# Performance work log

Measured on AMD Instinct MI355X. Metric: run time of the kernel, lower is better.

The kernel has to match this reference:

```python
import jax, jax.numpy as jnp
import numpy as np

INPUT_DIM = 1024
HIDDEN_DIM = 2048
NUM_BLOCKS = 8
BLOCK_SIZE = HIDDEN_DIM // NUM_BLOCKS
BATCH = 2048


def setup_inputs() -> dict:
    key = jax.random.key(0)
    ks = jax.random.split(key, 6)
    # PyTorch GRUCell init: uniform(-1/sqrt(hidden_size), 1/sqrt(hidden_size))
    bound = 1.0 / np.sqrt(BLOCK_SIZE)
    u = lambda k, shape: jax.random.uniform(k, shape, jnp.float32, -bound, bound)
    return {
        "input": jax.random.normal(ks[0], (BATCH, INPUT_DIM), jnp.float32),
        "hidden": jax.random.normal(ks[1], (BATCH, HIDDEN_DIM), jnp.float32),
        # stacked per-block GRUCell params (block-diagonal structure)
        "W_ih": u(ks[2], (NUM_BLOCKS, 3 * BLOCK_SIZE, INPUT_DIM)),
        "W_hh": u(ks[3], (NUM_BLOCKS, 3 * BLOCK_SIZE, BLOCK_SIZE)),
        "b_ih": u(ks[4], (NUM_BLOCKS, 3 * BLOCK_SIZE)),
        "b_hh": u(ks[5], (NUM_BLOCKS, 3 * BLOCK_SIZE)),
    }


def reference(input, hidden, W_ih, W_hh, b_ih, b_hh):
    B = input.shape[0]
    nb, g3, bs = W_hh.shape  # [num_blocks, 3*block_size, block_size]
    hb = hidden.reshape(B, nb, bs)                      # [B, nb, bs]
    # input-to-gate and hidden-to-gate projections, batched over blocks
    gi = jnp.einsum("bi,ngi->bng", input, W_ih) + b_ih  # [B, nb, 3*bs]
    gh = jnp.einsum("bns,ngs->bng", hb, W_hh) + b_hh    # [B, nb, 3*bs]
    i_r, i_z, i_n = jnp.split(gi, 3, axis=-1)
    h_r, h_z, h_n = jnp.split(gh, 3, axis=-1)
    r = jax.nn.sigmoid(i_r + h_r)
    z = jax.nn.sigmoid(i_z + h_z)
    n = jnp.tanh(i_n + r * h_n)
    new_h = (1.0 - z) * n + z * hb                      # [B, nb, bs]
    return new_h.reshape(B, nb * bs)
```

## Files before the change

### kernel.cpp

```cpp
#include <hip/hip_runtime.h>
#include <hip/hip_bf16.h>
#include <type_traits>

typedef __attribute__((ext_vector_type(4))) float f32x4;
typedef __attribute__((ext_vector_type(8))) short bf16x8;

template <int V> using ic = std::integral_constant<int, V>;

static constexpr int B_   = 2048;
static constexpr int IN_  = 1024;
static constexpr int HID_ = 2048;
static constexpr int NB_  = 8;
static constexpr int BS_  = 256;
static constexpr int G3_  = 768;

__device__ __forceinline__ unsigned cvtpk(float lo, float hi) {
  unsigned r;
  asm("v_cvt_pk_bf16_f32 %0, %1, %2" : "=v"(r) : "v"(lo), "v"(hi));
  return r;
}

__global__ __launch_bounds__(256, 2) void gru_mfma(
    const float* __restrict__ xf,
    const float* __restrict__ hf,
    const float* __restrict__ Wih,
    const float* __restrict__ Whh,
    const float* __restrict__ b_ih,
    const float* __restrict__ b_hh,
    float* __restrict__ out)
{
  __shared__ __align__(16) char lds[2][40960];

  const int t    = threadIdx.x;
  const int lane = t & 63;
  const int wid  = t >> 6;
  const int wm   = wid >> 1;
  const int wn   = wid & 1;

  const int bid = blockIdx.x;
  const int swz = (bid & 7) * 64 + (bid >> 3);
  const int mrow0 = (swz & 15) * 128;
  const int ct    = swz >> 4;
  const int n     = ct >> 2;
  const int s0    = (ct & 3) * 64;

  int arow[4], acol[4];
#pragma unroll
  for (int p = 0; p < 4; ++p) {
    int op = p * 4096 + t * 16;
    int ol = op ^ (((op >> 7) & 7) << 4);
    arow[p] = ol >> 7;
    acol[p] = (ol & 127) >> 1;
  }
  int wgrow[6], wcol[6];
#pragma unroll
  for (int q = 0; q < 6; ++q) {
    int op = q * 4096 + t * 16;
    int ol = op ^ (((op >> 7) & 7) << 4);
    int wr = ol >> 7;
    wgrow[q] = n * G3_ + (wr >> 6) * BS_ + s0 + (wr & 63);
    wcol[q]  = (ol & 127) >> 1;
  }

  f32x4 acc[4][4][2] = {};
  float4 s1[6][2];
  float4 s2[4][2];

  auto issueB1 = [&](int t2) {
#pragma unroll
    for (int p = 0; p < 4; ++p) {
      const float* src = (t2 < 16)
        ? xf + (size_t)(mrow0 + arow[p]) * IN_  + t2 * 64 + acol[p]
        : hf + (size_t)(mrow0 + arow[p]) * HID_ + n * BS_ + (t2 - 16) * 64 + acol[p];
      s1[p][0] = *reinterpret_cast<const float4*>(src);
      s1[p][1] = *reinterpret_cast<const float4*>(src + 4);
    }
#pragma unroll
    for (int q = 0; q < 2; ++q) {
      const float* src = (t2 < 16)
        ? Wih + (size_t)wgrow[q] * IN_ + t2 * 64 + wcol[q]
        : Whh + (size_t)wgrow[q] * BS_ + (t2 - 16) * 64 + wcol[q];
      s1[4 + q][0] = *reinterpret_cast<const float4*>(src);
      s1[4 + q][1] = *reinterpret_cast<const float4*>(src + 4);
    }
  };
  auto issueB2 = [&](int t2) {
#pragma unroll
    for (int j = 0; j < 4; ++j) {
      const int q = 2 + j;
      const float* src = (t2 < 16)
        ? Wih + (size_t)wgrow[q] * IN_ + t2 * 64 + wcol[q]
        : Whh + (size_t)wgrow[q] * BS_ + (t2 - 16) * 64 + wcol[q];
      s2[j][0] = *reinterpret_cast<const float4*>(src);
      s2[j][1] = *reinterpret_cast<const float4*>(src + 4);
    }
  };
  auto pack8 = [&](const float4& a, const float4& b) {
    union { unsigned u[4]; bf16x8 v; } r;
    r.u[0] = cvtpk(a.x, a.y); r.u[1] = cvtpk(a.z, a.w);
    r.u[2] = cvtpk(b.x, b.y); r.u[3] = cvtpk(b.z, b.w);
    return r.v;
  };
  auto writeB1 = [&](char* buf) {
#pragma unroll
    for (int p = 0; p < 4; ++p)
      *reinterpret_cast<bf16x8*>(buf + p * 4096 + t * 16) = pack8(s1[p][0], s1[p][1]);
#pragma unroll
    for (int q = 0; q < 2; ++q)
      *reinterpret_cast<bf16x8*>(buf + 16384 + q * 4096 + t * 16) = pack8(s1[4 + q][0], s1[4 + q][1]);
  };
  auto writeB2 = [&](char* buf) {
#pragma unroll
    for (int j = 0; j < 4; ++j)
      *reinterpret_cast<bf16x8*>(buf + 16384 + (2 + j) * 4096 + t * 16) = pack8(s2[j][0], s2[j][1]);
  };

  auto loadA = [&](const char* buf, bf16x8 (&af)[2][4]) {
#pragma unroll
    for (int ksub = 0; ksub < 2; ++ksub)
#pragma unroll
      for (int mi = 0; mi < 4; ++mi) {
        int ar  = wm * 64 + mi * 16 + (lane & 15);
        int off = ar * 128 + ksub * 64 + ((lane >> 4) * 16);
        off ^= (ar & 7) << 4;
        af[ksub][mi] = *reinterpret_cast<const bf16x8*>(buf + off);
      }
  };
  auto loadW = [&](const char* buf, int g, bf16x8 (&wf)[2][2]) {
#pragma unroll
    for (int ksub = 0; ksub < 2; ++ksub)
#pragma unroll
      for (int ni = 0; ni < 2; ++ni) {
        int wr  = g * 64 + wn * 32 + ni * 16 + (lane & 15);
        int off = wr * 128 + ksub * 64 + ((lane >> 4) * 16);
        off ^= (wr & 7) << 4;
        wf[ksub][ni] = *reinterpret_cast<const bf16x8*>(buf + 16384 + off);
      }
  };
  auto mfmaSet = [&](auto setc, bf16x8 (&af)[2][4], bf16x8 (&wf)[2][2]) {
    constexpr int set = decltype(setc)::value;
    __builtin_amdgcn_s_setprio(1);
#pragma unroll
    for (int ksub = 0; ksub < 2; ++ksub)
#pragma unroll
      for (int mi = 0; mi < 4; ++mi)
#pragma unroll
        for (int ni = 0; ni < 2; ++ni)
          acc[set][mi][ni] = __builtin_amdgcn_mfma_f32_16x16x32_bf16(
              af[ksub][mi], wf[ksub][ni], acc[set][mi][ni], 0, 0, 0);
    __builtin_amdgcn_s_setprio(0);
  };

  issueB1(0);
  writeB1((char*)lds[0]);
  issueB2(0);
  writeB2((char*)lds[0]);
  __syncthreads();

#pragma unroll
  for (int tt = 0; tt < 20; ++tt) {
    char* cur = (char*)lds[tt & 1];
    char* oth = (char*)lds[(tt & 1) ^ 1];
    bf16x8 af[2][4], wf[2][2];

    if (tt < 19) issueB1(tt + 1);
    __builtin_amdgcn_sched_barrier(0);
    loadA(cur, af);
    loadW(cur, 0, wf);
    mfmaSet(ic<0>{}, af, wf);
    __builtin_amdgcn_sched_barrier(0);
    if (tt < 19) { writeB1(oth); issueB2(tt + 1); }
    __builtin_amdgcn_sched_barrier(0);
    loadW(cur, 1, wf);
    mfmaSet(ic<1>{}, af, wf);
    loadW(cur, 2, wf);
    if (tt < 16) mfmaSet(ic<2>{}, af, wf);
    else         mfmaSet(ic<3>{}, af, wf);
    __builtin_amdgcn_sched_barrier(0);
    if (tt < 19) writeB2(oth);
    __syncthreads();
  }

#pragma unroll
  for (int ni = 0; ni < 2; ++ni) {
    int scol = s0 + wn * 32 + ni * 16 + (lane & 15);
    float br_i = b_ih[n * G3_ + 0 * BS_ + scol];
    float bz_i = b_ih[n * G3_ + 1 * BS_ + scol];
    float bn_i = b_ih[n * G3_ + 2 * BS_ + scol];
    float br_h = b_hh[n * G3_ + 0 * BS_ + scol];
    float bz_h = b_hh[n * G3_ + 1 * BS_ + scol];
    float bn_h = b_hh[n * G3_ + 2 * BS_ + scol];
    int gcol = n * BS_ + scol;
#pragma unroll
    for (int mi = 0; mi < 4; ++mi) {
#pragma unroll
      for (int i = 0; i < 4; ++i) {
        int row = mrow0 + wm * 64 + mi * 16 + (lane >> 4) * 4 + i;
        float hprev = hf[(size_t)row * HID_ + gcol];
        float rr = acc[0][mi][ni][i] + br_i + br_h;
        float zz = acc[1][mi][ni][i] + bz_i + bz_h;
        float r  = 1.f / (1.f + __expf(-rr));
        float z  = 1.f / (1.f + __expf(-zz));
        float ng = tanhf(acc[2][mi][ni][i] + bn_i + r * (acc[3][mi][ni][i] + bn_h));
        out[(size_t)row * HID_ + gcol] = (1.f - z) * ng + z * hprev;
      }
    }
  }
}

extern "C" void kernel_launch(void* const* d_in, const int* in_sizes, int n_in,
                              void* d_out, int out_size, void* d_ws, size_t ws_size,
                              hipStream_t stream) {
  const float* x   = (const float*)d_in[0];
  const float* h   = (const float*)d_in[1];
  const float* Wih = (const float*)d_in[2];
  const float* Whh = (const float*)d_in[3];
  const float* bih = (const float*)d_in[4];
  const float* bhh = (const float*)d_in[5];
  float* out = (float*)d_out;
  (void)d_ws; (void)ws_size;

  gru_mfma<<<512, 256, 0, stream>>>(x, h, Wih, Whh, bih, bhh, out);
}
```

Baseline: 55.60 us.

## Widen block tile to 128 hidden columns with 512 threads and LDS-staged epilogue

Each workgroup now covers 128 hidden columns per gate instead of 64. It uses 8 waves (512 threads) and half as many workgroups, so each staged input/hidden tile is reused across twice as many weight rows, reducing global and LDS traffic per output. The epilogue stages z and the candidate gate in per-wave LDS, then reads them back so that the hidden-state load and output store become row-contiguous float4 accesses. The trade-off is 128KB of LDS per workgroup, which likely limits each CU to one workgroup, and a grid of only 256 blocks, which leaves less latency hiding and more exposure to load imbalance.

```diff
diff --git a/kernel.cpp b/kernel.cpp
--- a/kernel.cpp
+++ b/kernel.cpp
@@ -20,7 +20,7 @@
   return r;
 }
 
-__global__ __launch_bounds__(256, 2) void gru_mfma(
+__global__ __launch_bounds__(512, 2) void gru_mfma(
     const float* __restrict__ xf,
     const float* __restrict__ hf,
     const float* __restrict__ Wih,
@@ -29,70 +29,69 @@
     const float* __restrict__ b_hh,
     float* __restrict__ out)
 {
-  __shared__ __align__(16) char lds[2][40960];
+  __shared__ __align__(16) char lds[2][65536];
 
   const int t    = threadIdx.x;
   const int lane = t & 63;
   const int wid  = t >> 6;
-  const int wm   = wid >> 1;
-  const int wn   = wid & 1;
+  const int wm   = wid >> 2;
+  const int wn   = wid & 3;
 
   const int bid = blockIdx.x;
-  const int swz = (bid & 7) * 64 + (bid >> 3);
+  const int swz = (bid & 7) * 32 + (bid >> 3);
   const int mrow0 = (swz & 15) * 128;
-  const int ct    = swz >> 4;
-  const int n     = ct >> 2;
-  const int s0    = (ct & 3) * 64;
-
-  int arow[4], acol[4];
-#pragma unroll
-  for (int p = 0; p < 4; ++p) {
-    int op = p * 4096 + t * 16;
+  const int ct2   = swz >> 4;
+  const int n     = ct2 >> 1;
+  const int s0    = (ct2 & 1) * 128;
+
+  int arow[2], acolE[2];
+#pragma unroll
+  for (int p = 0; p < 2; ++p) {
+    int op = p * 8192 + t * 16;
     int ol = op ^ (((op >> 7) & 7) << 4);
-    arow[p] = ol >> 7;
-    acol[p] = (ol & 127) >> 1;
-  }
-  int wgrow[6], wcol[6];
+    arow[p]  = ol >> 7;
+    acolE[p] = (ol & 127) >> 1;
+  }
+  int wgr[6], wcolE[6];
 #pragma unroll
   for (int q = 0; q < 6; ++q) {
-    int op = q * 4096 + t * 16;
+    int op = q * 8192 + t * 16;
     int ol = op ^ (((op >> 7) & 7) << 4);
     int wr = ol >> 7;
-    wgrow[q] = n * G3_ + (wr >> 6) * BS_ + s0 + (wr & 63);
-    wcol[q]  = (ol & 127) >> 1;
+    wgr[q]   = n * G3_ + (wr >> 7) * BS_ + s0 + (wr & 127);
+    wcolE[q] = (ol & 127) >> 1;
   }
 
   f32x4 acc[4][4][2] = {};
-  float4 s1[6][2];
-  float4 s2[4][2];
-
-  auto issueB1 = [&](int t2) {
-#pragma unroll
-    for (int p = 0; p < 4; ++p) {
-      const float* src = (t2 < 16)
-        ? xf + (size_t)(mrow0 + arow[p]) * IN_  + t2 * 64 + acol[p]
-        : hf + (size_t)(mrow0 + arow[p]) * HID_ + n * BS_ + (t2 - 16) * 64 + acol[p];
-      s1[p][0] = *reinterpret_cast<const float4*>(src);
-      s1[p][1] = *reinterpret_cast<const float4*>(src + 4);
+  float4 s[4][2];
+
+  auto issueB1 = [&](int tt) {
+#pragma unroll
+    for (int p = 0; p < 2; ++p) {
+      const float* src = (tt < 16)
+        ? xf + (size_t)(mrow0 + arow[p]) * IN_  + tt * 64 + acolE[p]
+        : hf + (size_t)(mrow0 + arow[p]) * HID_ + n * BS_ + (tt - 16) * 64 + acolE[p];
+      s[p][0] = *reinterpret_cast<const float4*>(src);
+      s[p][1] = *reinterpret_cast<const float4*>(src + 4);
     }
 #pragma unroll
     for (int q = 0; q < 2; ++q) {
-      const float* src = (t2 < 16)
-        ? Wih + (size_t)wgrow[q] * IN_ + t2 * 64 + wcol[q]
-        : Whh + (size_t)wgrow[q] * BS_ + (t2 - 16) * 64 + wcol[q];
-      s1[4 + q][0] = *reinterpret_cast<const float4*>(src);
-      s1[4 + q][1] = *reinterpret_cast<const float4*>(src + 4);
-    }
-  };
-  auto issueB2 = [&](int t2) {
+      const float* src = (tt < 16)
+        ? Wih + (size_t)wgr[q] * IN_ + tt * 64 + wcolE[q]
+        : Whh + (size_t)wgr[q] * BS_ + (tt - 16) * 64 + wcolE[q];
+      s[2 + q][0] = *reinterpret_cast<const float4*>(src);
+      s[2 + q][1] = *reinterpret_cast<const float4*>(src + 4);
+    }
+  };
+  auto issueB2 = [&](int tt) {
 #pragma unroll
     for (int j = 0; j < 4; ++j) {
       const int q = 2 + j;
-      const float* src = (t2 < 16)
-        ? Wih + (size_t)wgrow[q] * IN_ + t2 * 64 + wcol[q]
-        : Whh + (size_t)wgrow[q] * BS_ + (t2 - 16) * 64 + wcol[q];
-      s2[j][0] = *reinterpret_cast<const float4*>(src);
-      s2[j][1] = *reinterpret_cast<const float4*>(src + 4);
+      const float* src = (tt < 16)
+        ? Wih + (size_t)wgr[q] * IN_ + tt * 64 + wcolE[q]
+        : Whh + (size_t)wgr[q] * BS_ + (tt - 16) * 64 + wcolE[q];
+      s[j][0] = *reinterpret_cast<const float4*>(src);
+      s[j][1] = *reinterpret_cast<const float4*>(src + 4);
     }
   };
   auto pack8 = [&](const float4& a, const float4& b) {
@@ -101,21 +100,23 @@
     r.u[2] = cvtpk(b.x, b.y); r.u[3] = cvtpk(b.z, b.w);
     return r.v;
   };
-  auto writeB1 = [&](char* buf) {
-#pragma unroll
-    for (int p = 0; p < 4; ++p)
-      *reinterpret_cast<bf16x8*>(buf + p * 4096 + t * 16) = pack8(s1[p][0], s1[p][1]);
+  auto writeB1 = [&](int buf) {
+    char* base = (char*)lds[buf];
+#pragma unroll
+    for (int p = 0; p < 2; ++p)
+      *reinterpret_cast<bf16x8*>(base + p * 8192 + t * 16) = pack8(s[p][0], s[p][1]);
 #pragma unroll
     for (int q = 0; q < 2; ++q)
-      *reinterpret_cast<bf16x8*>(buf + 16384 + q * 4096 + t * 16) = pack8(s1[4 + q][0], s1[4 + q][1]);
-  };
-  auto writeB2 = [&](char* buf) {
+      *reinterpret_cast<bf16x8*>(base + 16384 + q * 8192 + t * 16) = pack8(s[2 + q][0], s[2 + q][1]);
+  };
+  auto writeB2 = [&](int buf) {
+    char* base = (char*)lds[buf] + 16384;
 #pragma unroll
     for (int j = 0; j < 4; ++j)
-      *reinterpret_cast<bf16x8*>(buf + 16384 + (2 + j) * 4096 + t * 16) = pack8(s2[j][0], s2[j][1]);
-  };
-
-  auto loadA = [&](const char* buf, bf16x8 (&af)[2][4]) {
+      *reinterpret_cast<bf16x8*>(base + (2 + j) * 8192 + t * 16) = pack8(s[j][0], s[j][1]);
+  };
+
+  auto loadA = [&](int buf, bf16x8 (&af)[2][4]) {
 #pragma unroll
     for (int ksub = 0; ksub < 2; ++ksub)
 #pragma unroll
@@ -123,87 +124,101 @@
         int ar  = wm * 64 + mi * 16 + (lane & 15);
         int off = ar * 128 + ksub * 64 + ((lane >> 4) * 16);
         off ^= (ar & 7) << 4;
-        af[ksub][mi] = *reinterpret_cast<const bf16x8*>(buf + off);
+        af[ksub][mi] = *reinterpret_cast<const bf16x8*>((const char*)lds[buf] + off);
       }
   };
-  auto loadW = [&](const char* buf, int g, bf16x8 (&wf)[2][2]) {
-#pragma unroll
-    for (int ksub = 0; ksub < 2; ++ksub)
+  auto gate = [&](int buf, int g, auto setc, bf16x8 (&af)[2][4]) {
+    constexpr int set = decltype(setc)::value;
+#pragma unroll
+    for (int ksub = 0; ksub < 2; ++ksub) {
+      bf16x8 wf[2];
 #pragma unroll
       for (int ni = 0; ni < 2; ++ni) {
-        int wr  = g * 64 + wn * 32 + ni * 16 + (lane & 15);
+        int wr  = g * 128 + wn * 32 + ni * 16 + (lane & 15);
         int off = wr * 128 + ksub * 64 + ((lane >> 4) * 16);
         off ^= (wr & 7) << 4;
-        wf[ksub][ni] = *reinterpret_cast<const bf16x8*>(buf + 16384 + off);
+        wf[ni] = *reinterpret_cast<const bf16x8*>((const char*)lds[buf] + 16384 + off);
       }
-  };
-  auto mfmaSet = [&](auto setc, bf16x8 (&af)[2][4], bf16x8 (&wf)[2][2]) {
-    constexpr int set = decltype(setc)::value;
-    __builtin_amdgcn_s_setprio(1);
-#pragma unroll
-    for (int ksub = 0; ksub < 2; ++ksub)
+      __builtin_amdgcn_s_setprio(1);
 #pragma unroll
       for (int mi = 0; mi < 4; ++mi)
 #pragma unroll
         for (int ni = 0; ni < 2; ++ni)
           acc[set][mi][ni] = __builtin_amdgcn_mfma_f32_16x16x32_bf16(
-              af[ksub][mi], wf[ksub][ni], acc[set][mi][ni], 0, 0, 0);
-    __builtin_amdgcn_s_setprio(0);
-  };
-
-  issueB1(0);
-  writeB1((char*)lds[0]);
-  issueB2(0);
-  writeB2((char*)lds[0]);
+              af[ksub][mi], wf[ni], acc[set][mi][ni], 0, 0, 0);
+      __builtin_amdgcn_s_setprio(0);
+    }
+  };
+
+  issueB1(0); writeB1(0);
+  issueB2(0); writeB2(0);
   __syncthreads();
 
 #pragma unroll
   for (int tt = 0; tt < 20; ++tt) {
-    char* cur = (char*)lds[tt & 1];
-    char* oth = (char*)lds[(tt & 1) ^ 1];
-    bf16x8 af[2][4], wf[2][2];
+    const int cur = tt & 1, oth = cur ^ 1;
+    bf16x8 af[2][4];
 
     if (tt < 19) issueB1(tt + 1);
     __builtin_amdgcn_sched_barrier(0);
     loadA(cur, af);
-    loadW(cur, 0, wf);
-    mfmaSet(ic<0>{}, af, wf);
+    gate(cur, 0, ic<0>{}, af);
     __builtin_amdgcn_sched_barrier(0);
     if (tt < 19) { writeB1(oth); issueB2(tt + 1); }
     __builtin_amdgcn_sched_barrier(0);
-    loadW(cur, 1, wf);
-    mfmaSet(ic<1>{}, af, wf);
-    loadW(cur, 2, wf);
-    if (tt < 16) mfmaSet(ic<2>{}, af, wf);
-    else         mfmaSet(ic<3>{}, af, wf);
+    gate(cur, 1, ic<1>{}, af);
+    if (tt < 16) gate(cur, 2, ic<2>{}, af);
+    else         gate(cur, 2, ic<3>{}, af);
     __builtin_amdgcn_sched_barrier(0);
     if (tt < 19) writeB2(oth);
     __syncthreads();
   }
 
-#pragma unroll
-  for (int ni = 0; ni < 2; ++ni) {
-    int scol = s0 + wn * 32 + ni * 16 + (lane & 15);
-    float br_i = b_ih[n * G3_ + 0 * BS_ + scol];
-    float bz_i = b_ih[n * G3_ + 1 * BS_ + scol];
-    float bn_i = b_ih[n * G3_ + 2 * BS_ + scol];
-    float br_h = b_hh[n * G3_ + 0 * BS_ + scol];
-    float bz_h = b_hh[n * G3_ + 1 * BS_ + scol];
-    float bn_h = b_hh[n * G3_ + 2 * BS_ + scol];
-    int gcol = n * BS_ + scol;
-#pragma unroll
-    for (int mi = 0; mi < 4; ++mi) {
+  float* ew = (float*)lds + wid * 1152;
+  const int gc0 = n * BS_ + s0 + wn * 32;
+
+#pragma unroll
+  for (int mi = 0; mi < 4; ++mi) {
+#pragma unroll
+    for (int ni = 0; ni < 2; ++ni) {
+      int scol = s0 + wn * 32 + ni * 16 + (lane & 15);
+      float br = b_ih[n * G3_ + 0 * BS_ + scol] + b_hh[n * G3_ + 0 * BS_ + scol];
+      float bzv = b_ih[n * G3_ + 1 * BS_ + scol] + b_hh[n * G3_ + 1 * BS_ + scol];
+      float bni = b_ih[n * G3_ + 2 * BS_ + scol];
+      float bnh = b_hh[n * G3_ + 2 * BS_ + scol];
 #pragma unroll
       for (int i = 0; i < 4; ++i) {
-        int row = mrow0 + wm * 64 + mi * 16 + (lane >> 4) * 4 + i;
-        float hprev = hf[(size_t)row * HID_ + gcol];
-        float rr = acc[0][mi][ni][i] + br_i + br_h;
-        float zz = acc[1][mi][ni][i] + bz_i + bz_h;
+        float rr = acc[0][mi][ni][i] + br;
+        float zz = acc[1][mi][ni][i] + bzv;
         float r  = 1.f / (1.f + __expf(-rr));
         float z  = 1.f / (1.f + __expf(-zz));
-        float ng = tanhf(acc[2][mi][ni][i] + bn_i + r * (acc[3][mi][ni][i] + bn_h));
-        out[(size_t)row * HID_ + gcol] = (1.f - z) * ng + z * hprev;
+        float ng = tanhf(acc[2][mi][ni][i] + bni + r * (acc[3][mi][ni][i] + bnh));
+        int lrow = (lane >> 4) * 4 + i;
+        int lcol = ni * 16 + (lane & 15);
+        ew[lrow * 36 + lcol]       = z;
+        ew[576 + lrow * 36 + lcol] = ng;
       }
+    }
+    asm volatile("s_waitcnt lgkmcnt(0)");
+    __builtin_amdgcn_sched_barrier(0);
+#pragma unroll
+    for (int p = 0; p < 2; ++p) {
+      int lrow = p * 8 + (lane >> 3);
+      int grow = mrow0 + wm * 64 + mi * 16 + lrow;
+      int cc   = (lane & 7) * 4;
+      float4 z4  = *reinterpret_cast<const float4*>(ew + lrow * 36 + cc);
+      float4 ng4 = *reinterpret_cast<const float4*>(ew + 576 + lrow * 36 + cc);
+      float4 h4  = *reinterpret_cast<const float4*>(hf + (size_t)grow * HID_ + gc0 + cc);
+      float4 o4;
+      o4.x = (1.f - z4.x) * ng4.x + z4.x * h4.x;
+      o4.y = (1.f - z4.y) * ng4.y + z4.y * h4.y;
+      o4.z = (1.f - z4.z) * ng4.z + z4.z * h4.z;
+      o4.w = (1.f - z4.w) * ng4.w + z4.w * h4.w;
+      *reinterpret_cast<float4*>(out + (size_t)grow * HID_ + gc0 + cc) = o4;
+    }
+    if (mi < 3) {
+      asm volatile("s_waitcnt lgkmcnt(0)");
+      __builtin_amdgcn_sched_barrier(0);
     }
   }
 }
@@ -220,5 +235,5 @@
   float* out = (float*)d_out;
   (void)d_ws; (void)ws_size;
 
-  gru_mfma<<<512, 256, 0, stream>>>(x, h, Wih, Whh, bih, bhh, out);
+  gru_mfma<<<256, 512, 0, stream>>>(x, h, Wih, Whh, bih, bhh, out);
 }
```

New measurement: 55.49 us. About the same (-0.2%).
